# Kernel optimization log

Measured on AMD Instinct MI355X. Metric: run time of the kernel, lower is better.

## Reference

```python
import jax, jax.numpy as jnp
import numpy as np

B, T, C, H = 4, 2048, 1024, 16
D = C // H  # head_dim = 64

def setup_inputs() -> dict:
    key = jax.random.key(0)
    k1, k2, k3 = jax.random.split(key, 3)
    x = jax.random.normal(k1, (B, T, C), dtype=jnp.float32)
    # Linear weights stored as (out_features, in_features) like torch; we apply x @ W.T
    w_attn = jax.random.normal(k2, (3 * C, C), dtype=jnp.float32) * (1.0 / np.sqrt(C))
    w_proj = jax.random.normal(k3, (C, C), dtype=jnp.float32) * (1.0 / np.sqrt(C))
    return {"x": x, "w_attn": w_attn, "w_proj": w_proj}

def reference(x, w_attn, w_proj):
    Bv, Tv, Cv = x.shape
    qkv = jnp.einsum('btc,fc->btf', x, w_attn)  # [B,T,3C]
    q, k, v = jnp.split(qkv, 3, axis=-1)
    # [B,H,T,D]
    q = q.reshape(Bv, Tv, H, D).transpose(0, 2, 1, 3)
    k = k.reshape(Bv, Tv, H, D).transpose(0, 2, 1, 3)
    v = v.reshape(Bv, Tv, H, D).transpose(0, 2, 1, 3)
    scale = 1.0 / np.sqrt(D).astype(np.float32)
    att = jnp.einsum('bhqd,bhkd->bhqk', q, k) * scale
    causal = jnp.tril(jnp.ones((Tv, Tv), dtype=bool))
    att = jnp.where(causal, att, -jnp.inf)
    att = jax.nn.softmax(att, axis=-1)
    y = jnp.einsum('bhqk,bhkd->bhqd', att, v)
    y = y.transpose(0, 2, 1, 3).reshape(Bv, Tv, Cv)
    return jnp.einsum('btc,oc->bto', y, w_proj)
```

## Files before the change

### kernel.cpp

```cpp
#include <hip/hip_runtime.h>
#include <cstdint>
#include <cstddef>

typedef __attribute__((ext_vector_type(8))) short short8;
typedef __attribute__((ext_vector_type(4))) float f32x4;
typedef unsigned int u32;

#define MFMA_BF16(a, b, c) __builtin_amdgcn_mfma_f32_16x16x32_bf16((a), (b), (c), 0, 0, 0)

__device__ __forceinline__ void async16(const void* g, void* l) {
  __builtin_amdgcn_global_load_lds(
      (const __attribute__((address_space(1))) u32*)g,
      (__attribute__((address_space(3))) u32*)l, 16, 0, 0);
}

__device__ __forceinline__ short f2bf(float f) {
  u32 u = __builtin_bit_cast(u32, f);
  u += 0x7fffu + ((u >> 16) & 1u);
  return (short)(u >> 16);
}

__device__ __forceinline__ u32 pack_bf16_trunc(float lo, float hi) {
  return __builtin_amdgcn_perm(__builtin_bit_cast(u32, hi),
                               __builtin_bit_cast(u32, lo), 0x07060302u);
}

__global__ __launch_bounds__(256) void cast_all_kernel(
    const float* __restrict__ x, const float* __restrict__ wa,
    const float* __restrict__ wp, short* __restrict__ xb,
    short* __restrict__ wab, short* __restrict__ wpb) {
  const int i = blockIdx.x * blockDim.x + threadIdx.x;
  const float4* src;
  short4* dst;
  float sc = 1.0f;
  if (i < 2097152) {
    src = (const float4*)x + i;
    dst = (short4*)xb + i;
  } else if (i < 2883584) {
    const int j = i - 2097152;
    if (j < 262144) sc = 0.18033688011112042f;
    src = (const float4*)wa + j;
    dst = (short4*)wab + j;
  } else {
    const int j = i - 2883584;
    src = (const float4*)wp + j;
    dst = (short4*)wpb + j;
  }
  float4 v = *src;
  short4 r;
  r.x = f2bf(v.x * sc); r.y = f2bf(v.y * sc);
  r.z = f2bf(v.z * sc); r.w = f2bf(v.w * sc);
  *dst = r;
}

template <bool OUT_BF16, bool V_FUSE>
__global__ __launch_bounds__(256) void gemm_bt_kernel(
    const short* __restrict__ A, const short* __restrict__ Bt,
    void* __restrict__ Cv, int M, int N, int K) {
  __shared__ __align__(16) short As[128 * 64];
  __shared__ __align__(16) short Bs[128 * 64];

  const int tid  = threadIdx.x;
  const int lane = tid & 63;
  const int wave = tid >> 6;
  const int quad = lane >> 4;
  const int l15  = lane & 15;

  const int id  = blockIdx.y * gridDim.x + blockIdx.x;
  const int xcd = id & 7;
  const int j   = id >> 3;
  const int by  = xcd * 8 + (j & 7);
  const int bx  = j >> 3;
  const int bm  = by * 128;
  const int bn  = bx * 128;

  const int wm = (wave >> 1) * 64;
  const int wn = (wave & 1) * 64;

  f32x4 acc[4][4];
#pragma unroll
  for (int i = 0; i < 4; ++i)
#pragma unroll
    for (int jj = 0; jj < 4; ++jj) acc[i][jj] = (f32x4){0.f, 0.f, 0.f, 0.f};

  int srow[4], scol[4];
#pragma unroll
  for (int it = 0; it < 4; ++it) {
    const int s = tid + it * 256;
    srow[it] = s >> 3;
    scol[it] = ((s & 7) ^ (srow[it] & 7)) * 8;
  }
  const int xk = l15 & 7;

  for (int k0 = 0; k0 < K; k0 += 64) {
    __syncthreads();
#pragma unroll
    for (int it = 0; it < 4; ++it) {
      const int s = tid + it * 256;
      async16(A  + (size_t)(bm + srow[it]) * K + k0 + scol[it], &As[s * 8]);
      async16(Bt + (size_t)(bn + srow[it]) * K + k0 + scol[it], &Bs[s * 8]);
    }
    __syncthreads();

    short8 af[4][2], bf[4][2];
#pragma unroll
    for (int mt = 0; mt < 4; ++mt) {
      const int ra = (wm + mt * 16 + l15) * 64;
      af[mt][0] = *(const short8*)&As[ra + ((quad) ^ xk) * 8];
      af[mt][1] = *(const short8*)&As[ra + ((4 + quad) ^ xk) * 8];
    }
#pragma unroll
    for (int nt = 0; nt < 4; ++nt) {
      const int rb = (wn + nt * 16 + l15) * 64;
      bf[nt][0] = *(const short8*)&Bs[rb + ((quad) ^ xk) * 8];
      bf[nt][1] = *(const short8*)&Bs[rb + ((4 + quad) ^ xk) * 8];
    }
#pragma unroll
    for (int kk = 0; kk < 2; ++kk)
#pragma unroll
      for (int mt = 0; mt < 4; ++mt)
#pragma unroll
        for (int nt = 0; nt < 4; ++nt)
          acc[mt][nt] = MFMA_BF16(af[mt][kk], bf[nt][kk], acc[mt][nt]);
  }

  if (V_FUSE && bn >= 2048) {
    const int b   = bm >> 11;
    const int btt = bm & 2047;
#pragma unroll
    for (int mt = 0; mt < 4; ++mt) {
      const int tt   = btt + wm + mt * 16;
      const int kt   = tt >> 6;
      const int t64b = (tt & 63) + quad * 4;
      const int kkb  = t64b >> 5;
      const int q16  = (t64b >> 3) & 3;
      const int jb   = t64b & 7;
#pragma unroll
      for (int nt = 0; nt < 4; ++nt) {
        const int dcol = bn - 2048 + wn + nt * 16;
        const int h  = dcol >> 6;
        const int dt = (dcol >> 4) & 3;
        short* dst = (short*)Cv +
            (size_t)(b * 2048 + kt * 64 + h * 4 + dt) * 3072 + 2048 +
            kkb * 512 + (q16 * 16 + l15) * 8 + jb;
        u32 w0 = (u32)(unsigned short)f2bf(acc[mt][nt][0]) |
                 ((u32)(unsigned short)f2bf(acc[mt][nt][1]) << 16);
        u32 w1 = (u32)(unsigned short)f2bf(acc[mt][nt][2]) |
                 ((u32)(unsigned short)f2bf(acc[mt][nt][3]) << 16);
        *(uint2*)dst = make_uint2(w0, w1);
      }
    }
  } else {
#pragma unroll
    for (int mt = 0; mt < 4; ++mt) {
      const int r0e = bm + wm + mt * 16 + quad * 4;
#pragma unroll
      for (int nt = 0; nt < 4; ++nt) {
        const int c = bn + wn + nt * 16 + l15;
#pragma unroll
        for (int reg = 0; reg < 4; ++reg) {
          float v = acc[mt][nt][reg];
          if (OUT_BF16)
            ((short*)Cv)[(size_t)(r0e + reg) * N + c] = f2bf(v);
          else
            ((float*)Cv)[(size_t)(r0e + reg) * N + c] = v;
        }
      }
    }
  }
}

__global__ __launch_bounds__(256, 4) void attn_kernel(
    const short* __restrict__ qkv, short* __restrict__ y) {
  __shared__ __align__(16) short Ks[2][4096];
  __shared__ __align__(16) short Ps[4][1024];

  const int bh    = blockIdx.x;
  const int pairi = blockIdx.y;
  const int b = bh >> 4, h = bh & 15;
  const int tid  = threadIdx.x;
  const int lane = tid & 63;
  const int wave = tid >> 6;
  const int quad = lane >> 4, l15 = lane & 15;
  const int base_row = b * 2048;
  short* Pw = &Ps[wave][0];

  const int s0 = tid, s1 = tid + 256;
  const int r0s = s0 >> 3, c0s = (s0 & 7) ^ (r0s & 7);
  const int r1s = s1 >> 3, c1s = (s1 & 7) ^ (r1s & 7);
  const short* kbase0 = qkv + (size_t)(base_row + r0s) * 3072 + 1024 + h * 64 + c0s * 8;
  const short* kbase1 = qkv + (size_t)(base_row + r1s) * 3072 + 1024 + h * 64 + c1s * 8;

  const short* vbaseA = qkv + ((size_t)base_row + h * 4) * 3072 + 2048 +
                        (size_t)lane * 8;

  const int xk = l15 & 7;

  for (int half = 0; half < 2; ++half) {
    const int qi  = half ? (31 - pairi) : pairi;
    const int nkt = qi + 1;
    const int qg0 = qi * 64 + wave * 16;

    short8 qf[2];
    {
      const short* qp = qkv +
          (size_t)(base_row + qg0 + l15) * 3072 + h * 64 + quad * 8;
      qf[0] = *(const short8*)qp;
      qf[1] = *(const short8*)(qp + 32);
    }
    float l_r = 0.f;
    f32x4 o[4];
#pragma unroll
    for (int dt = 0; dt < 4; ++dt) o[dt] = (f32x4){0.f, 0.f, 0.f, 0.f};

    async16(kbase0, &Ks[0][s0 * 8]);
    async16(kbase1, &Ks[0][s1 * 8]);

    for (int kt = 0; kt < nkt; ++kt) {
      const int kvb = kt * 64;
      __syncthreads();

      if (kt + 1 < nkt) {
        const int nb = (kt + 1) & 1;
        const size_t koff = (size_t)(kvb + 64) * 3072;
        async16(kbase0 + koff, &Ks[nb][s0 * 8]);
        async16(kbase1 + koff, &Ks[nb][s1 * 8]);
      }
      const short* Kb = &Ks[kt & 1][0];

      const short* vp = vbaseA + (size_t)kt * 64 * 3072;
      short8 vf[4][2];
#pragma unroll
      for (int dt = 0; dt < 4; ++dt) {
        vf[dt][0] = *(const short8*)(vp + (size_t)dt * 3072);
        vf[dt][1] = *(const short8*)(vp + (size_t)dt * 3072 + 512);
      }

      short8 kf[4][2];
#pragma unroll
      for (int nt = 0; nt < 4; ++nt) {
        kf[nt][0] = *(const short8*)&Kb[(nt * 16 + l15) * 64 + ((quad) ^ xk) * 8];
        kf[nt][1] = *(const short8*)&Kb[(nt * 16 + l15) * 64 + ((4 + quad) ^ xk) * 8];
      }

      f32x4 s[4];
#pragma unroll
      for (int nt = 0; nt < 4; ++nt) {
        s[nt] = MFMA_BF16(kf[nt][0], qf[0], ((f32x4){0.f, 0.f, 0.f, 0.f}));
        s[nt] = MFMA_BF16(kf[nt][1], qf[1], s[nt]);
      }

      float p[4][4];
      if (kvb + 64 <= qg0) {
#pragma unroll
        for (int nt = 0; nt < 4; ++nt)
#pragma unroll
          for (int r = 0; r < 4; ++r)
            p[nt][r] = __builtin_amdgcn_exp2f(s[nt][r]);
      } else {
        const int qrel = qg0 + l15 - kvb;
#pragma unroll
        for (int nt = 0; nt < 4; ++nt)
#pragma unroll
          for (int r = 0; r < 4; ++r) {
            const int kvl = nt * 16 + quad * 4 + r;
            p[nt][r] = (kvl <= qrel) ? __builtin_amdgcn_exp2f(s[nt][r]) : 0.f;
          }
      }

      float rs = ((p[0][0] + p[0][1]) + (p[0][2] + p[0][3])) +
                 ((p[1][0] + p[1][1]) + (p[1][2] + p[1][3])) +
                 ((p[2][0] + p[2][1]) + (p[2][2] + p[2][3])) +
                 ((p[3][0] + p[3][1]) + (p[3][2] + p[3][3]));
      rs += __shfl_xor(rs, 16);
      rs += __shfl_xor(rs, 32);
      l_r += rs;

#pragma unroll
      for (int nt = 0; nt < 4; ++nt) {
        u32 w0 = pack_bf16_trunc(p[nt][0], p[nt][1]);
        u32 w1 = pack_bf16_trunc(p[nt][2], p[nt][3]);
        const int p0 = 8 * nt + 2 * quad;
        u32* dst = (u32*)Pw + (p0 >> 4) * 256 + ((p0 >> 2) & 3) * 64 +
                   l15 * 4 + (p0 & 3);
        *(uint2*)dst = make_uint2(w0, w1);
      }
      short8 pf0 = *(const short8*)&Pw[quad * 128 + l15 * 8];
      short8 pf1 = *(const short8*)&Pw[512 + quad * 128 + l15 * 8];

#pragma unroll
      for (int dt = 0; dt < 4; ++dt) {
        o[dt] = MFMA_BF16(vf[dt][0], pf0, o[dt]);
        o[dt] = MFMA_BF16(vf[dt][1], pf1, o[dt]);
      }
    }

    {
      const float inv = 1.f / l_r;
#pragma unroll
      for (int dt = 0; dt < 4; ++dt) {
        const int d = dt * 16 + quad * 4;
        u32 w0 = pack_bf16_trunc(o[dt][0] * inv, o[dt][1] * inv);
        u32 w1 = pack_bf16_trunc(o[dt][2] * inv, o[dt][3] * inv);
        *(uint2*)&Pw[(d >> 5) * 512 + l15 * 32 + (d & 31)] = make_uint2(w0, w1);
      }
      const int qq = lane >> 2, ck = lane & 3;
      const size_t yrow = (size_t)(base_row + qg0 + qq);
#pragma unroll
      for (int kkd = 0; kkd < 2; ++kkd) {
        short8 vv = *(const short8*)&Pw[kkd * 512 + qq * 32 + ck * 8];
        *(short8*)(y + yrow * 1024 + h * 64 + kkd * 32 + ck * 8) = vv;
      }
    }
    __syncthreads();
  }
}

extern "C" void kernel_launch(void* const* d_in, const int* in_sizes, int n_in,
                              void* d_out, int out_size, void* d_ws,
                              size_t ws_size, hipStream_t stream) {
  const float* x  = (const float*)d_in[0];
  const float* wa = (const float*)d_in[1];
  const float* wp = (const float*)d_in[2];
  float* out = (float*)d_out;

  char* ws = (char*)d_ws;
  short* xb  = (short*)(ws + 0);
  short* wab = (short*)(ws + 16777216);
  short* wpb = (short*)(ws + 23068672);
  short* qkv = (short*)(ws + 25165824);
  short* yb  = (short*)(ws + 75497472);

  cast_all_kernel<<<12288, 256, 0, stream>>>(x, wa, wp, xb, wab, wpb);

  gemm_bt_kernel<true, true><<<dim3(3072 / 128, 8192 / 128), 256, 0, stream>>>(
      xb, wab, (void*)qkv, 8192, 3072, 1024);

  attn_kernel<<<dim3(64, 16), 256, 0, stream>>>(qkv, yb);

  gemm_bt_kernel<false, false><<<dim3(1024 / 128, 8192 / 128), 256, 0, stream>>>(
      yb, wpb, (void*)out, 8192, 1024, 1024);
}
```

Before: 226.7 us.

## Add dedicated QKV GEMM kernel with 256x128 tiles and 4-stage async pipeline

Replaces the generic GEMM for the QKV projection with a specialized 512-thread kernel using 256x128 block tiles, K-step 32, and a 4-buffer LDS ring with two stages of async global-to-LDS prefetch in flight. It also adds XCD-aware block remapping and raises wave priority around the MFMA section. The aim is to hide global load latency and improve data reuse in the largest GEMM. The cost is more LDS per block (96KB), which caps occupancy at one or two blocks per CU, and the shape is hardcoded.

```diff
diff --git a/kernel.cpp b/kernel.cpp
--- a/kernel.cpp
+++ b/kernel.cpp
@@ -53,7 +53,127 @@
   *dst = r;
 }
 
-template <bool OUT_BF16, bool V_FUSE>
+__global__ __launch_bounds__(512, 2) void gemm1_kernel(
+    const short* __restrict__ A, const short* __restrict__ Bt,
+    short* __restrict__ C) {
+  __shared__ __align__(16) short As[4][8192];
+  __shared__ __align__(16) short Bs[4][4096];
+
+  const int tid  = threadIdx.x;
+  const int lane = tid & 63;
+  const int wave = tid >> 6;
+  const int quad = lane >> 4;
+  const int l15  = lane & 15;
+
+  const int id = blockIdx.y * 24 + blockIdx.x;
+  const int g  = (id & 7) * 96 + (id >> 3);
+  const int by = g / 24;
+  const int bx = g - by * 24;
+  const int bm = by * 256;
+  const int bn = bx * 128;
+
+  const int wm = (wave >> 1) * 64;
+  const int wn = (wave & 1) * 64;
+
+  f32x4 acc[4][4];
+#pragma unroll
+  for (int m = 0; m < 4; ++m)
+#pragma unroll
+    for (int n = 0; n < 4; ++n) acc[m][n] = (f32x4){0.f, 0.f, 0.f, 0.f};
+
+  const int srow = tid >> 2;
+  const int c8   = ((tid & 3) ^ ((tid >> 3) & 3)) * 8;
+  const short* pa0 = A  + (size_t)(bm + srow) * 1024 + c8;
+  const short* pa1 = pa0 + (size_t)128 * 1024;
+  const short* pb  = Bt + (size_t)(bn + srow) * 1024 + c8;
+  const int dA0 = tid * 8, dA1 = (tid + 512) * 8, dB = tid * 8;
+
+#define STAGE3(T)                                  \
+  do {                                             \
+    const int o_ = (T) * 32;                       \
+    const int b_ = (T) & 3;                        \
+    async16(pa0 + o_, &As[b_][dA0]);               \
+    async16(pa1 + o_, &As[b_][dA1]);               \
+    async16(pb  + o_, &Bs[b_][dB]);                \
+  } while (0)
+
+  STAGE3(0);
+  STAGE3(1);
+
+  const int fu = (quad ^ ((l15 >> 1) & 3)) * 8;
+
+  for (int t = 0; t < 32; ++t) {
+    if (t == 31) {
+      asm volatile("s_waitcnt vmcnt(0)" ::: "memory");
+    } else {
+      asm volatile("s_waitcnt vmcnt(3)" ::: "memory");
+    }
+    if (t + 2 < 32) STAGE3(t + 2);
+    __builtin_amdgcn_sched_barrier(0);
+    __builtin_amdgcn_s_barrier();
+
+    const short* Ab = &As[t & 3][0];
+    const short* Bb = &Bs[t & 3][0];
+    short8 af[4], bf[4];
+#pragma unroll
+    for (int m = 0; m < 4; ++m)
+      af[m] = *(const short8*)&Ab[(wm + m * 16 + l15) * 32 + fu];
+#pragma unroll
+    for (int n = 0; n < 4; ++n)
+      bf[n] = *(const short8*)&Bb[(wn + n * 16 + l15) * 32 + fu];
+
+    __builtin_amdgcn_s_setprio(1);
+#pragma unroll
+    for (int m = 0; m < 4; ++m)
+#pragma unroll
+      for (int n = 0; n < 4; ++n)
+        acc[m][n] = MFMA_BF16(af[m], bf[n], acc[m][n]);
+    __builtin_amdgcn_s_setprio(0);
+  }
+#undef STAGE3
+
+  if (bn >= 2048) {
+    const int b   = bm >> 11;
+    const int btt = bm & 2047;
+#pragma unroll
+    for (int mt = 0; mt < 4; ++mt) {
+      const int tt   = btt + wm + mt * 16;
+      const int kt   = tt >> 6;
+      const int t64b = (tt & 63) + quad * 4;
+      const int kkb  = t64b >> 5;
+      const int q16  = (t64b >> 3) & 3;
+      const int jb   = t64b & 7;
+#pragma unroll
+      for (int nt = 0; nt < 4; ++nt) {
+        const int dcol = bn - 2048 + wn + nt * 16;
+        const int h  = dcol >> 6;
+        const int dt = (dcol >> 4) & 3;
+        short* dst = C +
+            (size_t)(b * 2048 + kt * 64 + h * 4 + dt) * 3072 + 2048 +
+            kkb * 512 + (q16 * 16 + l15) * 8 + jb;
+        u32 w0 = (u32)(unsigned short)f2bf(acc[mt][nt][0]) |
+                 ((u32)(unsigned short)f2bf(acc[mt][nt][1]) << 16);
+        u32 w1 = (u32)(unsigned short)f2bf(acc[mt][nt][2]) |
+                 ((u32)(unsigned short)f2bf(acc[mt][nt][3]) << 16);
+        *(uint2*)dst = make_uint2(w0, w1);
+      }
+    }
+  } else {
+#pragma unroll
+    for (int mt = 0; mt < 4; ++mt) {
+      const int r0e = bm + wm + mt * 16 + quad * 4;
+#pragma unroll
+      for (int nt = 0; nt < 4; ++nt) {
+        const int c = bn + wn + nt * 16 + l15;
+#pragma unroll
+        for (int reg = 0; reg < 4; ++reg)
+          C[(size_t)(r0e + reg) * 3072 + c] = f2bf(acc[mt][nt][reg]);
+      }
+    }
+  }
+}
+
+template <bool OUT_BF16>
 __global__ __launch_bounds__(256) void gemm_bt_kernel(
     const short* __restrict__ A, const short* __restrict__ Bt,
     void* __restrict__ Cv, int M, int N, int K) {
@@ -124,47 +244,19 @@
           acc[mt][nt] = MFMA_BF16(af[mt][kk], bf[nt][kk], acc[mt][nt]);
   }
 
-  if (V_FUSE && bn >= 2048) {
-    const int b   = bm >> 11;
-    const int btt = bm & 2047;
-#pragma unroll
-    for (int mt = 0; mt < 4; ++mt) {
-      const int tt   = btt + wm + mt * 16;
-      const int kt   = tt >> 6;
-      const int t64b = (tt & 63) + quad * 4;
-      const int kkb  = t64b >> 5;
-      const int q16  = (t64b >> 3) & 3;
-      const int jb   = t64b & 7;
-#pragma unroll
-      for (int nt = 0; nt < 4; ++nt) {
-        const int dcol = bn - 2048 + wn + nt * 16;
-        const int h  = dcol >> 6;
-        const int dt = (dcol >> 4) & 3;
-        short* dst = (short*)Cv +
-            (size_t)(b * 2048 + kt * 64 + h * 4 + dt) * 3072 + 2048 +
-            kkb * 512 + (q16 * 16 + l15) * 8 + jb;
-        u32 w0 = (u32)(unsigned short)f2bf(acc[mt][nt][0]) |
-                 ((u32)(unsigned short)f2bf(acc[mt][nt][1]) << 16);
-        u32 w1 = (u32)(unsigned short)f2bf(acc[mt][nt][2]) |
-                 ((u32)(unsigned short)f2bf(acc[mt][nt][3]) << 16);
-        *(uint2*)dst = make_uint2(w0, w1);
-      }
-    }
-  } else {
-#pragma unroll
-    for (int mt = 0; mt < 4; ++mt) {
-      const int r0e = bm + wm + mt * 16 + quad * 4;
-#pragma unroll
-      for (int nt = 0; nt < 4; ++nt) {
-        const int c = bn + wn + nt * 16 + l15;
-#pragma unroll
-        for (int reg = 0; reg < 4; ++reg) {
-          float v = acc[mt][nt][reg];
-          if (OUT_BF16)
-            ((short*)Cv)[(size_t)(r0e + reg) * N + c] = f2bf(v);
-          else
-            ((float*)Cv)[(size_t)(r0e + reg) * N + c] = v;
-        }
+#pragma unroll
+  for (int mt = 0; mt < 4; ++mt) {
+    const int r0e = bm + wm + mt * 16 + quad * 4;
+#pragma unroll
+    for (int nt = 0; nt < 4; ++nt) {
+      const int c = bn + wn + nt * 16 + l15;
+#pragma unroll
+      for (int reg = 0; reg < 4; ++reg) {
+        float v = acc[mt][nt][reg];
+        if (OUT_BF16)
+          ((short*)Cv)[(size_t)(r0e + reg) * N + c] = f2bf(v);
+        else
+          ((float*)Cv)[(size_t)(r0e + reg) * N + c] = v;
       }
     }
   }
@@ -333,11 +425,10 @@
 
   cast_all_kernel<<<12288, 256, 0, stream>>>(x, wa, wp, xb, wab, wpb);
 
-  gemm_bt_kernel<true, true><<<dim3(3072 / 128, 8192 / 128), 256, 0, stream>>>(
-      xb, wab, (void*)qkv, 8192, 3072, 1024);
+  gemm1_kernel<<<dim3(24, 32), 512, 0, stream>>>(xb, wab, qkv);
 
   attn_kernel<<<dim3(64, 16), 256, 0, stream>>>(qkv, yb);
 
-  gemm_bt_kernel<false, false><<<dim3(1024 / 128, 8192 / 128), 256, 0, stream>>>(
+  gemm_bt_kernel<false><<<dim3(1024 / 128, 8192 / 128), 256, 0, stream>>>(
       yb, wpb, (void*)out, 8192, 1024, 1024);
 }
```

New measurement: 238.1 us. 5.0% more time.
